# Kernel optimization log

Hardware: AMD Instinct MI355X
Metric: run time of the kernel (lower is better)

Reference implementation:

```python
import jax, jax.numpy as jnp
import numpy as np

B, H, S, D = 2, 16, 2048, 64  # batch, heads, seq (n_qry == n_tok), head_dim


def setup_inputs() -> dict:
    key = jax.random.key(0)
    kq, kk, kv = jax.random.split(key, 3)
    Q = jax.random.normal(kq, (B, H, S, D), dtype=jnp.float32)
    K_cache = jax.random.normal(kk, (B, H, S, D), dtype=jnp.float32)
    V_cache = jax.random.normal(kv, (B, H, S, D), dtype=jnp.float32)
    return {"Q": Q, "K_cache": K_cache, "V_cache": V_cache}


def reference(Q, K_cache, V_cache):
    n_qry = Q.shape[-2]
    n_tok = K_cache.shape[-2]
    scale = 1.0 / jnp.sqrt(jnp.asarray(Q.shape[-1], Q.dtype))
    # [B, H, n_qry, n_tok] scores
    A = jnp.einsum('bhqd,bhkd->bhqk', Q, K_cache) * scale
    # causal mask: query q may attend key k iff k <= q + (n_tok - n_qry)
    q_idx = jnp.arange(n_qry)[:, None]
    k_idx = jnp.arange(n_tok)[None, :]
    mask = k_idx <= q_idx + (n_tok - n_qry)
    A = jnp.where(mask, A, -jnp.inf)
    P = jax.nn.softmax(A, axis=-1)
    return jnp.einsum('bhqk,bhkd->bhqd', P, V_cache)
```

## Files before the change

### kernel.cpp

```cpp
#include <hip/hip_runtime.h>

typedef __attribute__((ext_vector_type(8))) short bf16x8;
typedef __attribute__((ext_vector_type(4))) float f32x4;

#define NB 2
#define NH 16
#define NS 2048
#define ND 64
#define NBH 32
#define QSCALE (0.125f * 1.44269504088896f)
#define CMAX 12.0f

static __device__ __forceinline__ unsigned pack2(float lo, float hi) {
  return __builtin_amdgcn_perm(__builtin_bit_cast(unsigned, hi),
                               __builtin_bit_cast(unsigned, lo), 0x07060302u);
}


__global__ __launch_bounds__(256) void prep_kernel(const float* __restrict__ K,
                                                   const float* __restrict__ V,
                                                   short* __restrict__ W) {
  const int xcd = blockIdx.x & 7;
  const int rest = blockIdx.x >> 3;
  const int lb = rest >> 5;
  const int kb = rest & 31;
  const int bh = xcd * 4 + lb;
  const float* Kp = K + (size_t)bh * NS * ND + (size_t)kb * 64 * ND;
  const float* Vp = V + (size_t)bh * NS * ND + (size_t)kb * 64 * ND;
  short* Wp = W + ((size_t)bh * 32 + kb) * 8192;

  __shared__ float vt[64 * 65];

  {
    int vrow = threadIdx.x >> 2, seg = threadIdx.x & 3;
    const float* src = Vp + vrow * ND + seg * 16;
    float* dst = vt + vrow * 65 + seg * 16;
#pragma unroll
    for (int i = 0; i < 4; ++i) {
      float4 v = *(const float4*)(src + i * 4);
      dst[i * 4 + 0] = v.x; dst[i * 4 + 1] = v.y;
      dst[i * 4 + 2] = v.z; dst[i * 4 + 3] = v.w;
    }
  }

#pragma unroll
  for (int e0 = 0; e0 < 512; e0 += 256) {
    int e = e0 + threadIdx.x;
    int c = e >> 6, lane = e & 63;
    int st = c >> 1, cc = c & 1, quad = lane >> 4, col = lane & 15;
    int prow = 32 * (st >> 1) + 8 * (col >> 2) + 4 * (st & 1) + (col & 3);
    const float* kr = Kp + prow * ND + cc * 32 + quad * 8;
    float4 a = *(const float4*)kr;
    float4 b = *(const float4*)(kr + 4);
    uint4 u = {pack2(a.x, a.y), pack2(a.z, a.w), pack2(b.x, b.y), pack2(b.z, b.w)};
    *(uint4*)(Wp + (size_t)e * 8) = u;
  }
  __syncthreads();

#pragma unroll
  for (int e0 = 0; e0 < 512; e0 += 256) {
    int e = e0 + threadIdx.x;
    int c = e >> 6, lane = e & 63;
    int g = c >> 2, t = c & 3, quad = lane >> 4, col = lane & 15;
    const float* base = vt + (32 * g + 8 * quad) * 65 + t * 16 + col;
    float f[8];
#pragma unroll
    for (int j = 0; j < 8; ++j) f[j] = base[j * 65];
    uint4 u = {pack2(f[0], f[1]), pack2(f[2], f[3]),
               pack2(f[4], f[5]), pack2(f[6], f[7])};
    *(uint4*)(Wp + 4096 + (size_t)e * 8) = u;
  }
}

__global__ __launch_bounds__(256, 2) void fa_kernel(
    const float* __restrict__ Q, const short* __restrict__ W,
    float* __restrict__ O) {
  const int lane = threadIdx.x & 63;
  const int wave = threadIdx.x >> 6;
  const int col  = lane & 15;
  const int quad = lane >> 4;

  const int i = blockIdx.x;
  const int xcd = i & 7;
  const int j = i >> 3;
  const int phase = j >> 5;
  const int slot = j & 31;
  const int bh = xcd * 4 + (slot & 3);
  const int rblk = slot >> 2;
  const int r = phase ? (15 - rblk) : rblk;
  const int qg = r * 4 + wave;
  const int T = (qg >> 1) + 1;

  const float* Qp = Q + (size_t)bh * NS * ND;
  const short* Wb = W + (size_t)bh * 32 * 8192;
  float*       Op = O + (size_t)bh * NS * ND;

  bf16x8 qf[2][2];
#pragma unroll
  for (int f = 0; f < 2; ++f) {
    const float* qrow = Qp + (size_t)(qg * 32 + f * 16 + col) * ND + quad * 8;
#pragma unroll
    for (int c = 0; c < 2; ++c) {
      float4 a = *(const float4*)(qrow + c * 32);
      float4 b = *(const float4*)(qrow + c * 32 + 4);
      union { bf16x8 v; unsigned u[4]; } t;
      t.u[0] = pack2(a.x * QSCALE, a.y * QSCALE);
      t.u[1] = pack2(a.z * QSCALE, a.w * QSCALE);
      t.u[2] = pack2(b.x * QSCALE, b.y * QSCALE);
      t.u[3] = pack2(b.z * QSCALE, b.w * QSCALE);
      qf[f][c] = t.v;
    }
  }

  f32x4 o4[2][4];
#pragma unroll
  for (int f = 0; f < 2; ++f)
#pragma unroll
    for (int t = 0; t < 4; ++t) o4[f][t] = (f32x4){0.f, 0.f, 0.f, 0.f};
  float lsum[2] = {0.f, 0.f};

  auto computeTile = [&](const bf16x8 (&kf)[8], const short* base, bool last) {
    bf16x8 vr[8];
#pragma unroll
    for (int c = 0; c < 8; ++c)
      vr[c] = *(const bf16x8*)(base + 4096 + c * 512 + lane * 8);

    float sc[2][4][4];
#pragma unroll
    for (int st = 0; st < 4; ++st) {
#pragma unroll
      for (int f = 0; f < 2; ++f) {
        f32x4 acc = (f32x4){-CMAX, -CMAX, -CMAX, -CMAX};
        acc = __builtin_amdgcn_mfma_f32_16x16x32_bf16(kf[st * 2 + 0], qf[f][0],
                                                      acc, 0, 0, 0);
        acc = __builtin_amdgcn_mfma_f32_16x16x32_bf16(kf[st * 2 + 1], qf[f][1],
                                                      acc, 0, 0, 0);
#pragma unroll
        for (int rr = 0; rr < 4; ++rr) sc[f][st][rr] = acc[rr];
      }
    }

    if (last) {
#pragma unroll
      for (int f = 0; f < 2; ++f) {
        int qrel = (qg & 1) * 32 + f * 16 + col;
#pragma unroll
        for (int st = 0; st < 4; ++st)
#pragma unroll
          for (int rr = 0; rr < 4; ++rr) {
            int phys = 32 * (st >> 1) + 8 * quad + 4 * (st & 1) + rr;
            if (phys > qrel) sc[f][st][rr] = -INFINITY;
          }
      }
    }

    bf16x8 pf[2][2];
#pragma unroll
    for (int f = 0; f < 2; ++f)
#pragma unroll
      for (int g = 0; g < 2; ++g) {
        float p0 = __builtin_amdgcn_exp2f(sc[f][2 * g + 0][0]);
        float p1 = __builtin_amdgcn_exp2f(sc[f][2 * g + 0][1]);
        float p2 = __builtin_amdgcn_exp2f(sc[f][2 * g + 0][2]);
        float p3 = __builtin_amdgcn_exp2f(sc[f][2 * g + 0][3]);
        float p4 = __builtin_amdgcn_exp2f(sc[f][2 * g + 1][0]);
        float p5 = __builtin_amdgcn_exp2f(sc[f][2 * g + 1][1]);
        float p6 = __builtin_amdgcn_exp2f(sc[f][2 * g + 1][2]);
        float p7 = __builtin_amdgcn_exp2f(sc[f][2 * g + 1][3]);
        lsum[f] += ((p0 + p1) + (p2 + p3)) + ((p4 + p5) + (p6 + p7));
        union { bf16x8 v; unsigned u[4]; } tt;
        tt.u[0] = pack2(p0, p1);
        tt.u[1] = pack2(p2, p3);
        tt.u[2] = pack2(p4, p5);
        tt.u[3] = pack2(p6, p7);
        pf[f][g] = tt.v;
      }

#pragma unroll
    for (int g = 0; g < 2; ++g)
#pragma unroll
      for (int t4 = 0; t4 < 4; ++t4) {
#pragma unroll
        for (int f = 0; f < 2; ++f)
          o4[f][t4] = __builtin_amdgcn_mfma_f32_16x16x32_bf16(
              pf[f][g], vr[g * 4 + t4], o4[f][t4], 0, 0, 0);
      }
  };

  bf16x8 ka[8], kb[8];
#pragma unroll
  for (int c = 0; c < 8; ++c)
    ka[c] = *(const bf16x8*)(Wb + c * 512 + lane * 8);

  for (int t = 0; t < T; t += 2) {
    const short* base0 = Wb + (size_t)t * 8192;
    if (t + 1 < T) {
#pragma unroll
      for (int c = 0; c < 8; ++c)
        kb[c] = *(const bf16x8*)(base0 + 8192 + c * 512 + lane * 8);
    }
    computeTile(ka, base0, t == T - 1);
    if (t + 1 < T) {
      const short* base1 = base0 + 8192;
      if (t + 2 < T) {
#pragma unroll
        for (int c = 0; c < 8; ++c)
          ka[c] = *(const bf16x8*)(base1 + 8192 + c * 512 + lane * 8);
      }
      computeTile(kb, base1, t + 1 == T - 1);
    }
  }

#pragma unroll
  for (int f = 0; f < 2; ++f) {
    float lt = lsum[f];
    lt += __shfl_xor(lt, 16, 64);
    lt += __shfl_xor(lt, 32, 64);
#pragma unroll
    for (int rr = 0; rr < 4; ++rr) {
      float lr = __shfl(lt, quad * 4 + rr, 64);
      float inv = 1.0f / lr;
      float* orow = Op + (size_t)(qg * 32 + f * 16 + quad * 4 + rr) * ND + col;
#pragma unroll
      for (int t4 = 0; t4 < 4; ++t4) orow[t4 * 16] = o4[f][t4][rr] * inv;
    }
  }
}

extern "C" void kernel_launch(void* const* d_in, const int* in_sizes, int n_in,
                              void* d_out, int out_size, void* d_ws, size_t ws_size,
                              hipStream_t stream) {
  const float* Q = (const float*)d_in[0];
  const float* K = (const float*)d_in[1];
  const float* V = (const float*)d_in[2];
  short* W = (short*)d_ws;
  hipLaunchKernelGGL(prep_kernel, dim3(NBH * 32), dim3(256), 0, stream, K, V, W);
  hipLaunchKernelGGL(fa_kernel, dim3(512), dim3(256), 0, stream, Q, W,
                     (float*)d_out);
}
```

Baseline: 118.6 us.

## Split causal attention into key-range pieces with LDS staging and combine pass

Replaces the per-wave full key sweep with a split-K decomposition. Each block handles one 256-query tile against a piece of four 64-key tiles, giving 36 uniform-work pieces per head. K/V tiles are staged into shared memory via async global-to-LDS loads with double buffering, so all four waves share the loads. Unnormalized partial outputs and row sums go to workspace, and a new combine kernel sums the pieces and normalizes. This targets load imbalance from causal triangles and redundant K/V loads per wave, at the cost of an extra kernel launch, partial-result traffic, and block-wide barriers.

```diff
diff --git a/kernel.cpp b/kernel.cpp
--- a/kernel.cpp
+++ b/kernel.cpp
@@ -10,6 +10,7 @@
 #define NBH 32
 #define QSCALE (0.125f * 1.44269504088896f)
 #define CMAX 12.0f
+#define PART_STRIDE 16640
 
 static __device__ __forceinline__ unsigned pack2(float lo, float hi) {
   return __builtin_amdgcn_perm(__builtin_bit_cast(unsigned, hi),
@@ -74,7 +75,7 @@
 
 __global__ __launch_bounds__(256, 2) void fa_kernel(
     const float* __restrict__ Q, const short* __restrict__ W,
-    float* __restrict__ O) {
+    float* __restrict__ P) {
   const int lane = threadIdx.x & 63;
   const int wave = threadIdx.x >> 6;
   const int col  = lane & 15;
@@ -82,23 +83,45 @@
 
   const int i = blockIdx.x;
   const int xcd = i & 7;
-  const int j = i >> 3;
-  const int phase = j >> 5;
-  const int slot = j & 31;
-  const int bh = xcd * 4 + (slot & 3);
-  const int rblk = slot >> 2;
-  const int r = phase ? (15 - rblk) : rblk;
-  const int qg = r * 4 + wave;
-  const int T = (qg >> 1) + 1;
+  const int rest = i >> 3;
+  const int bh = xcd * 4 + (rest & 3);
+  const int pc = rest >> 2;
+  int qt = 0;
+#pragma unroll
+  for (int q = 1; q <= 7; ++q)
+    if (pc >= (q * (q + 1)) / 2) qt = q;
+  const int piece = pc - (qt * (qt + 1)) / 2;
+  const int kt0 = piece * 4;
+  const int qbase = qt * 256 + wave * 64;
+  const int wlim = qt * 4 + wave;
+
+  __shared__ short Kbuf[2][4096];
+  __shared__ short Vbuf[2][4096];
 
   const float* Qp = Q + (size_t)bh * NS * ND;
   const short* Wb = W + (size_t)bh * 32 * 8192;
-  float*       Op = O + (size_t)bh * NS * ND;
-
-  bf16x8 qf[2][2];
-#pragma unroll
-  for (int f = 0; f < 2; ++f) {
-    const float* qrow = Qp + (size_t)(qg * 32 + f * 16 + col) * ND + quad * 8;
+
+  auto stage = [&](int kt, int b) {
+    const short* base = Wb + (size_t)kt * 8192;
+#pragma unroll
+    for (int ii = 0; ii < 4; ++ii) {
+      int id = wave * 4 + ii;
+      const short* g = base + id * 512 + lane * 8;
+      __attribute__((address_space(3))) void* dst =
+          (id < 8)
+              ? (__attribute__((address_space(3))) void*)&Kbuf[b][id * 512]
+              : (__attribute__((address_space(3))) void*)&Vbuf[b][(id - 8) * 512];
+      __builtin_amdgcn_global_load_lds(
+          (const __attribute__((address_space(1))) void*)g, dst, 16, 0, 0);
+    }
+  };
+
+  stage(kt0, 0);
+
+  bf16x8 qf[4][2];
+#pragma unroll
+  for (int f = 0; f < 4; ++f) {
+    const float* qrow = Qp + (size_t)(qbase + f * 16 + col) * ND + quad * 8;
 #pragma unroll
     for (int c = 0; c < 2; ++c) {
       float4 a = *(const float4*)(qrow + c * 32);
@@ -112,119 +135,130 @@
     }
   }
 
-  f32x4 o4[2][4];
-#pragma unroll
-  for (int f = 0; f < 2; ++f)
+  f32x4 o4[4][4];
+#pragma unroll
+  for (int f = 0; f < 4; ++f)
 #pragma unroll
     for (int t = 0; t < 4; ++t) o4[f][t] = (f32x4){0.f, 0.f, 0.f, 0.f};
-  float lsum[2] = {0.f, 0.f};
-
-  auto computeTile = [&](const bf16x8 (&kf)[8], const short* base, bool last) {
-    bf16x8 vr[8];
-#pragma unroll
-    for (int c = 0; c < 8; ++c)
-      vr[c] = *(const bf16x8*)(base + 4096 + c * 512 + lane * 8);
-
-    float sc[2][4][4];
-#pragma unroll
-    for (int st = 0; st < 4; ++st) {
-#pragma unroll
-      for (int f = 0; f < 2; ++f) {
-        f32x4 acc = (f32x4){-CMAX, -CMAX, -CMAX, -CMAX};
-        acc = __builtin_amdgcn_mfma_f32_16x16x32_bf16(kf[st * 2 + 0], qf[f][0],
-                                                      acc, 0, 0, 0);
-        acc = __builtin_amdgcn_mfma_f32_16x16x32_bf16(kf[st * 2 + 1], qf[f][1],
-                                                      acc, 0, 0, 0);
-#pragma unroll
-        for (int rr = 0; rr < 4; ++rr) sc[f][st][rr] = acc[rr];
+  float lsum[4] = {0.f, 0.f, 0.f, 0.f};
+
+#pragma unroll
+  for (int s = 0; s < 4; ++s) {
+    __syncthreads();
+    if (s + 1 < 4) stage(kt0 + s + 1, (s + 1) & 1);
+    const int ktg = kt0 + s;
+
+    if (ktg <= wlim) {
+      bf16x8 kf[8], vf[8];
+#pragma unroll
+      for (int c = 0; c < 8; ++c) {
+        kf[c] = *(const bf16x8*)&Kbuf[s & 1][c * 512 + lane * 8];
+        vf[c] = *(const bf16x8*)&Vbuf[s & 1][c * 512 + lane * 8];
       }
-    }
-
-    if (last) {
-#pragma unroll
-      for (int f = 0; f < 2; ++f) {
-        int qrel = (qg & 1) * 32 + f * 16 + col;
-#pragma unroll
-        for (int st = 0; st < 4; ++st)
-#pragma unroll
-          for (int rr = 0; rr < 4; ++rr) {
-            int phys = 32 * (st >> 1) + 8 * quad + 4 * (st & 1) + rr;
-            if (phys > qrel) sc[f][st][rr] = -INFINITY;
-          }
+      const bool diag = (ktg == wlim);
+
+#pragma unroll
+      for (int f = 0; f < 4; ++f) {
+        float sc[4][4];
+#pragma unroll
+        for (int st = 0; st < 4; ++st) {
+          f32x4 acc = (f32x4){-CMAX, -CMAX, -CMAX, -CMAX};
+          acc = __builtin_amdgcn_mfma_f32_16x16x32_bf16(kf[st * 2 + 0],
+                                                        qf[f][0], acc, 0, 0, 0);
+          acc = __builtin_amdgcn_mfma_f32_16x16x32_bf16(kf[st * 2 + 1],
+                                                        qf[f][1], acc, 0, 0, 0);
+#pragma unroll
+          for (int rr = 0; rr < 4; ++rr) sc[st][rr] = acc[rr];
+        }
+        if (diag) {
+          int qrel = f * 16 + col;
+#pragma unroll
+          for (int st = 0; st < 4; ++st)
+#pragma unroll
+            for (int rr = 0; rr < 4; ++rr) {
+              int phys = 32 * (st >> 1) + 8 * quad + 4 * (st & 1) + rr;
+              if (phys > qrel) sc[st][rr] = -INFINITY;
+            }
+        }
+        bf16x8 pf[2];
+#pragma unroll
+        for (int g = 0; g < 2; ++g) {
+          float p0 = __builtin_amdgcn_exp2f(sc[2 * g + 0][0]);
+          float p1 = __builtin_amdgcn_exp2f(sc[2 * g + 0][1]);
+          float p2 = __builtin_amdgcn_exp2f(sc[2 * g + 0][2]);
+          float p3 = __builtin_amdgcn_exp2f(sc[2 * g + 0][3]);
+          float p4 = __builtin_amdgcn_exp2f(sc[2 * g + 1][0]);
+          float p5 = __builtin_amdgcn_exp2f(sc[2 * g + 1][1]);
+          float p6 = __builtin_amdgcn_exp2f(sc[2 * g + 1][2]);
+          float p7 = __builtin_amdgcn_exp2f(sc[2 * g + 1][3]);
+          lsum[f] += ((p0 + p1) + (p2 + p3)) + ((p4 + p5) + (p6 + p7));
+          union { bf16x8 v; unsigned u[4]; } tt;
+          tt.u[0] = pack2(p0, p1);
+          tt.u[1] = pack2(p2, p3);
+          tt.u[2] = pack2(p4, p5);
+          tt.u[3] = pack2(p6, p7);
+          pf[g] = tt.v;
+        }
+#pragma unroll
+        for (int g = 0; g < 2; ++g)
+#pragma unroll
+          for (int t4 = 0; t4 < 4; ++t4)
+            o4[f][t4] = __builtin_amdgcn_mfma_f32_16x16x32_bf16(
+                pf[g], vf[g * 4 + t4], o4[f][t4], 0, 0, 0);
       }
     }
-
-    bf16x8 pf[2][2];
-#pragma unroll
-    for (int f = 0; f < 2; ++f)
-#pragma unroll
-      for (int g = 0; g < 2; ++g) {
-        float p0 = __builtin_amdgcn_exp2f(sc[f][2 * g + 0][0]);
-        float p1 = __builtin_amdgcn_exp2f(sc[f][2 * g + 0][1]);
-        float p2 = __builtin_amdgcn_exp2f(sc[f][2 * g + 0][2]);
-        float p3 = __builtin_amdgcn_exp2f(sc[f][2 * g + 0][3]);
-        float p4 = __builtin_amdgcn_exp2f(sc[f][2 * g + 1][0]);
-        float p5 = __builtin_amdgcn_exp2f(sc[f][2 * g + 1][1]);
-        float p6 = __builtin_amdgcn_exp2f(sc[f][2 * g + 1][2]);
-        float p7 = __builtin_amdgcn_exp2f(sc[f][2 * g + 1][3]);
-        lsum[f] += ((p0 + p1) + (p2 + p3)) + ((p4 + p5) + (p6 + p7));
-        union { bf16x8 v; unsigned u[4]; } tt;
-        tt.u[0] = pack2(p0, p1);
-        tt.u[1] = pack2(p2, p3);
-        tt.u[2] = pack2(p4, p5);
-        tt.u[3] = pack2(p6, p7);
-        pf[f][g] = tt.v;
-      }
-
-#pragma unroll
-    for (int g = 0; g < 2; ++g)
-#pragma unroll
-      for (int t4 = 0; t4 < 4; ++t4) {
-#pragma unroll
-        for (int f = 0; f < 2; ++f)
-          o4[f][t4] = __builtin_amdgcn_mfma_f32_16x16x32_bf16(
-              pf[f][g], vr[g * 4 + t4], o4[f][t4], 0, 0, 0);
-      }
-  };
-
-  bf16x8 ka[8], kb[8];
-#pragma unroll
-  for (int c = 0; c < 8; ++c)
-    ka[c] = *(const bf16x8*)(Wb + c * 512 + lane * 8);
-
-  for (int t = 0; t < T; t += 2) {
-    const short* base0 = Wb + (size_t)t * 8192;
-    if (t + 1 < T) {
-#pragma unroll
-      for (int c = 0; c < 8; ++c)
-        kb[c] = *(const bf16x8*)(base0 + 8192 + c * 512 + lane * 8);
-    }
-    computeTile(ka, base0, t == T - 1);
-    if (t + 1 < T) {
-      const short* base1 = base0 + 8192;
-      if (t + 2 < T) {
-#pragma unroll
-        for (int c = 0; c < 8; ++c)
-          ka[c] = *(const bf16x8*)(base1 + 8192 + c * 512 + lane * 8);
-      }
-      computeTile(kb, base1, t + 1 == T - 1);
-    }
-  }
-
-#pragma unroll
-  for (int f = 0; f < 2; ++f) {
+  }
+
+  float* pb = P + (size_t)(bh * 36 + pc) * PART_STRIDE;
+#pragma unroll
+  for (int f = 0; f < 4; ++f) {
+#pragma unroll
+    for (int rr = 0; rr < 4; ++rr) {
+      int rowq = wave * 64 + f * 16 + quad * 4 + rr;
+#pragma unroll
+      for (int t4 = 0; t4 < 4; ++t4)
+        pb[rowq * 64 + t4 * 16 + col] = o4[f][t4][rr];
+    }
     float lt = lsum[f];
     lt += __shfl_xor(lt, 16, 64);
     lt += __shfl_xor(lt, 32, 64);
-#pragma unroll
-    for (int rr = 0; rr < 4; ++rr) {
-      float lr = __shfl(lt, quad * 4 + rr, 64);
-      float inv = 1.0f / lr;
-      float* orow = Op + (size_t)(qg * 32 + f * 16 + quad * 4 + rr) * ND + col;
-#pragma unroll
-      for (int t4 = 0; t4 < 4; ++t4) orow[t4 * 16] = o4[f][t4][rr] * inv;
-    }
-  }
+    if (quad == 0) pb[16384 + wave * 64 + f * 16 + col] = lt;
+  }
+}
+
+__global__ __launch_bounds__(256) void comb_kernel(const float* __restrict__ P,
+                                                   float* __restrict__ O) {
+  const int i = blockIdx.x;
+  const int xcd = i & 7;
+  const int rest = i >> 3;
+  const int bh = xcd * 4 + (rest & 3);
+  const int rg = rest >> 2;
+  const int q0 = rg * 32;
+  const int qt = q0 >> 8;
+  const int np = qt + 1;
+  const int t = threadIdx.x;
+  const int row = t >> 3;
+  const int dof = (t & 7) * 8;
+  const int qloc = (q0 & 255) + row;
+
+  const float* pb =
+      P + (size_t)(bh * 36 + (qt * (qt + 1)) / 2) * PART_STRIDE;
+  float4 a = {0.f, 0.f, 0.f, 0.f}, b = {0.f, 0.f, 0.f, 0.f};
+  float lt = 0.f;
+  for (int p = 0; p < np; ++p) {
+    const float* pp = pb + (size_t)p * PART_STRIDE;
+    float4 x = *(const float4*)(pp + qloc * 64 + dof);
+    float4 y = *(const float4*)(pp + qloc * 64 + dof + 4);
+    a.x += x.x; a.y += x.y; a.z += x.z; a.w += x.w;
+    b.x += y.x; b.y += y.y; b.z += y.z; b.w += y.w;
+    lt += pp[16384 + qloc];
+  }
+  float inv = 1.0f / lt;
+  float* o = O + ((size_t)bh * NS + q0 + row) * ND + dof;
+  float4 ra = {a.x * inv, a.y * inv, a.z * inv, a.w * inv};
+  float4 rb = {b.x * inv, b.y * inv, b.z * inv, b.w * inv};
+  *(float4*)o = ra;
+  *(float4*)(o + 4) = rb;
 }
 
 extern "C" void kernel_launch(void* const* d_in, const int* in_sizes, int n_in,
@@ -234,7 +268,9 @@
   const float* K = (const float*)d_in[1];
   const float* V = (const float*)d_in[2];
   short* W = (short*)d_ws;
+  float* P = (float*)((char*)d_ws + 16777216);
   hipLaunchKernelGGL(prep_kernel, dim3(NBH * 32), dim3(256), 0, stream, K, V, W);
-  hipLaunchKernelGGL(fa_kernel, dim3(512), dim3(256), 0, stream, Q, W,
+  hipLaunchKernelGGL(fa_kernel, dim3(1152), dim3(256), 0, stream, Q, W, P);
+  hipLaunchKernelGGL(comb_kernel, dim3(2048), dim3(256), 0, stream, P,
                      (float*)d_out);
 }
```

After: 132.5 us. 11.7% more time.
